# Kernel optimization log

Measured on AMD Instinct MI355X. Metric: run time of the kernel, lower is better.

The kernel has to match this reference:

```python
import jax, jax.numpy as jnp
import numpy as np

B, T, N, M, P, YD = 256, 64, 128, 256, 256, 1


def lstm_cell(x, h, c, Wih, Whh, bih, bhh):
    # torch LSTM gate order: i, f, g, o
    gates = x @ Wih.T + h @ Whh.T + bih + bhh  # (B, 4H)
    i, f, g, o = jnp.split(gates, 4, axis=-1)
    c_new = jax.nn.sigmoid(f) * c + jax.nn.sigmoid(i) * jnp.tanh(g)
    h_new = jax.nn.sigmoid(o) * jnp.tanh(c_new)
    return h_new, c_new


def setup_inputs() -> dict:
    key = jax.random.key(0)
    ks = jax.random.split(key, 20)
    s = 0.05
    return {
        "inputs": jax.random.normal(ks[0], (B, T, N + YD), jnp.float32),
        "WU_e": jax.random.normal(ks[1], (T, 2 * M + T), jnp.float32) * s,
        "v_e": jax.random.normal(ks[2], (1, T), jnp.float32) * s,
        "Wih_e": jax.random.normal(ks[3], (4 * M, N), jnp.float32) * s,
        "Whh_e": jax.random.normal(ks[4], (4 * M, M), jnp.float32) * s,
        "bih_e": jax.random.normal(ks[5], (4 * M,), jnp.float32) * s,
        "bhh_e": jax.random.normal(ks[6], (4 * M,), jnp.float32) * s,
        "WU_d": jax.random.normal(ks[7], (M, 2 * P + M), jnp.float32) * s,
        "v_d": jax.random.normal(ks[8], (1, M), jnp.float32) * s,
        "wb_tilde": jax.random.normal(ks[9], (1, YD + M), jnp.float32) * s,
        "Wih_d": jax.random.normal(ks[10], (4 * P, 1), jnp.float32) * s,
        "Whh_d": jax.random.normal(ks[11], (4 * P, P), jnp.float32) * s,
        "bih_d": jax.random.normal(ks[12], (4 * P,), jnp.float32) * s,
        "bhh_d": jax.random.normal(ks[13], (4 * P,), jnp.float32) * s,
        "Wb_W": jax.random.normal(ks[14], (P, P + M), jnp.float32) * s,
        "Wb_b": jax.random.normal(ks[15], (P,), jnp.float32) * s,
        "vb_W": jax.random.normal(ks[16], (YD, P), jnp.float32) * s,
        "vb_b": jax.random.normal(ks[17], (YD,), jnp.float32) * s,
    }


def _darnn(inputs, WU_e, v_e, Wih_e, Whh_e, bih_e, bhh_e,
           WU_d, v_d, wb_tilde, Wih_d, Whh_d, bih_d, bhh_d,
           Wb_W, Wb_b, vb_W, vb_b):
    X = inputs[:, :, :N]          # (B, T, N)
    Y = inputs[:, :, N:]          # (B, T, YD)
    X_nt = jnp.transpose(X, (0, 2, 1))  # (B, N, T), constant across encoder steps

    # ---------------- Encoder ----------------
    def enc_step(carry, x_t):  # x_t: (B, N)
        h, c = carry
        hs = jnp.concatenate([h, c], axis=-1)  # (B, 2M)
        feat = jnp.concatenate(
            [jnp.broadcast_to(hs[:, None, :], (B, N, 2 * M)), X_nt], axis=-1)  # (B, N, 2M+T)
        E = (jnp.tanh(feat @ WU_e.T) @ v_e.T)[..., 0]  # (B, N)
        alpha = jax.nn.softmax(E, axis=1)
        h, c = lstm_cell(x_t * alpha, h, c, Wih_e, Whh_e, bih_e, bhh_e)
        return (h, c), h

    h0 = jnp.zeros((B, M), inputs.dtype)
    c0 = jnp.zeros((B, M), inputs.dtype)
    _, X_encoded = jax.lax.scan(enc_step, (h0, c0), jnp.transpose(X, (1, 0, 2)))
    Xe_bm = jnp.transpose(X_encoded, (1, 0, 2))  # (B, T, M)

    # ---------------- Decoder ----------------
    def dec_step(carry, y_t):  # y_t: (B, YD)
        h, c, _ = carry
        hs = jnp.concatenate([h, c], axis=-1)  # (B, 2P)
        feat = jnp.concatenate(
            [jnp.broadcast_to(hs[:, None, :], (B, T, 2 * P)), Xe_bm], axis=-1)  # (B, T, 2P+M)
        l = (jnp.tanh(feat @ WU_d.T) @ v_d.T)[..., 0]  # (B, T)
        beta = jax.nn.softmax(l, axis=1)
        ctx = jnp.einsum('bt,btm->bm', beta, Xe_bm)  # (B, M)
        y_tilde = jnp.concatenate([y_t, ctx], axis=-1) @ wb_tilde.T  # (B, 1)
        h, c = lstm_cell(y_tilde, h, c, Wih_d, Whh_d, bih_d, bhh_d)
        return (h, c, ctx), None

    hd0 = jnp.zeros((B, P), inputs.dtype)
    cd0 = jnp.zeros((B, P), inputs.dtype)
    ctx0 = jnp.zeros((B, M), inputs.dtype)
    (h, c, ctx), _ = jax.lax.scan(
        dec_step, (hd0, cd0, ctx0), jnp.transpose(Y[:, :T - 1, :], (1, 0, 2)))

    hidden = jnp.concatenate([h, ctx], axis=-1) @ Wb_W.T + Wb_b  # (B, P)
    y_hat = hidden @ vb_W.T + vb_b  # (B, YD)
    return y_hat


def reference(inputs, WU_e, v_e, Wih_e, Whh_e, bih_e, bhh_e,
              WU_d, v_d, wb_tilde, Wih_d, Whh_d, bih_d, bhh_d,
              Wb_W, Wb_b, vb_W, vb_b):
    return _darnn(inputs, WU_e, v_e, Wih_e, Whh_e, bih_e, bhh_e,
                  WU_d, v_d, wb_tilde, Wih_d, Whh_d, bih_d, bhh_d,
                  Wb_W, Wb_b, vb_W, vb_b)
```

## Files before the change

kernel.cpp:

```cpp
#include <hip/hip_runtime.h>
#include <math.h>


#define OFF_XWT   0u
#define OFF_XEWT  2097152u
#define OFF_XE    6291456u
#define OFF_HE    10485760u
#define OFF_HD    10616832u
#define OFF_SB    10747904u
#define OFF_SDB   10780672u
#define OFF_XA    10911744u
#define OFF_CTX   10944512u
#define OFF_YT    11010048u
#define OFF_BAR   11010304u
#define WS_END    11010816u

#define SLAB_F 24576
#define PER_F  2432
#define SCR_F  12288
#define SMEM_F (SLAB_F + PER_F + SCR_F)
#define SMEM_BYTES (SMEM_F * 4)

__device__ __forceinline__ float fast_tanh(float x) {
  float xc = fminf(15.f, fmaxf(-15.f, x));
  float e = __expf(2.f * xc);
  return 1.f - 2.f * __builtin_amdgcn_rcpf(e + 1.f);
}
__device__ __forceinline__ float fast_sig(float x) {
  float xc = fminf(30.f, fmaxf(-30.f, x));
  return __builtin_amdgcn_rcpf(1.f + __expf(-xc));
}
__device__ __forceinline__ float wave_max(float v) {
#pragma unroll
  for (int o = 32; o; o >>= 1) v = fmaxf(v, __shfl_xor(v, o));
  return v;
}
__device__ __forceinline__ float wave_sum(float v) {
#pragma unroll
  for (int o = 32; o; o >>= 1) v += __shfl_xor(v, o);
  return v;
}
__device__ __forceinline__ float dot4(float4 a, float4 b) {
  return a.x*b.x + a.y*b.y + a.z*b.z + a.w*b.w;
}

__device__ __forceinline__ void st1_sc1(float* p, float v) {
  asm volatile("global_store_dword %0, %1, off sc1" :: "v"(p), "v"(v) : "memory");
}
__device__ __forceinline__ void ld1q_sc1(float4& a, const float* pa) {
  asm volatile("global_load_dwordx4 %0, %1, off sc1\n\ts_waitcnt vmcnt(0)"
               : "=&v"(a) : "v"(pa) : "memory");
}
__device__ __forceinline__ void ld1q_nw(float4& a, const float* pa) {
  asm volatile("global_load_dwordx4 %0, %1, off sc1"
               : "=&v"(a) : "v"(pa) : "memory");
}
__device__ __forceinline__ void vm0() {
  asm volatile("s_waitcnt vmcnt(0)" ::: "memory");
}
__device__ __forceinline__ float ld1s_sc1(const float* p) {
  float v;
  asm volatile("global_load_dword %0, %1, off sc1\n\ts_waitcnt vmcnt(0)"
               : "=&v"(v) : "v"(p) : "memory");
  return v;
}
__device__ __forceinline__ void ld8s_sc1(
    float& a0,float& a1,float& a2,float& a3,float& a4,float& a5,float& a6,float& a7,
    const float* p0,const float* p1,const float* p2,const float* p3,
    const float* p4,const float* p5,const float* p6,const float* p7) {
  asm volatile(
      "global_load_dword %0, %8, off sc1\n\t"
      "global_load_dword %1, %9, off sc1\n\t"
      "global_load_dword %2, %10, off sc1\n\t"
      "global_load_dword %3, %11, off sc1\n\t"
      "global_load_dword %4, %12, off sc1\n\t"
      "global_load_dword %5, %13, off sc1\n\t"
      "global_load_dword %6, %14, off sc1\n\t"
      "global_load_dword %7, %15, off sc1\n\t"
      "s_waitcnt vmcnt(0)"
      : "=&v"(a0),"=&v"(a1),"=&v"(a2),"=&v"(a3),
        "=&v"(a4),"=&v"(a5),"=&v"(a6),"=&v"(a7)
      : "v"(p0),"v"(p1),"v"(p2),"v"(p3),"v"(p4),"v"(p5),"v"(p6),"v"(p7)
      : "memory");
}
__device__ __forceinline__ void atomic_add_sc1(float* p, float v) {
  asm volatile("global_atomic_add_f32 %0, %1, off sc1" :: "v"(p), "v"(v) : "memory");
}

#define FMA16V(a0,a1,a2,a3,xv,wv) \
  a0.x += xv.x*wv.x; a0.y += xv.x*wv.y; a0.z += xv.x*wv.z; a0.w += xv.x*wv.w; \
  a1.x += xv.y*wv.x; a1.y += xv.y*wv.y; a1.z += xv.y*wv.z; a1.w += xv.y*wv.w; \
  a2.x += xv.z*wv.x; a2.y += xv.z*wv.y; a2.z += xv.z*wv.z; a2.w += xv.z*wv.w; \
  a3.x += xv.w*wv.x; a3.y += xv.w*wv.y; a3.z += xv.w*wv.z; a3.w += xv.w*wv.w;

__device__ __forceinline__ void bar_arrive(unsigned* bar) {
  asm volatile("s_waitcnt vmcnt(0)" ::: "memory");
  __syncthreads();
  if (threadIdx.x == 0)
    __hip_atomic_fetch_add(bar, 1u, __ATOMIC_RELAXED, __HIP_MEMORY_SCOPE_AGENT);
}
__device__ __forceinline__ void bar_wait(unsigned* bar, unsigned target) {
  if (threadIdx.x == 0) {
    unsigned cur;
    do {
      cur = __hip_atomic_load(bar, __ATOMIC_RELAXED, __HIP_MEMORY_SCOPE_AGENT);
    } while (cur < target);
  }
  __syncthreads();
}

__global__ void darnn_init(float* __restrict__ ws, float* __restrict__ out) {
  unsigned i = blockIdx.x * 256u + threadIdx.x;
  const unsigned span = WS_END - OFF_HE;
  for (unsigned idx = i; idx < span; idx += gridDim.x * 256u) ws[OFF_HE + idx] = 0.f;
  if (i < 256u) out[i] = 0.f;
}

__global__ __launch_bounds__(512, 2) void darnn_main(
    const float* __restrict__ in,   const float* __restrict__ WUe,   const float* __restrict__ ve,
    const float* __restrict__ Wih_e,const float* __restrict__ Whh_e,
    const float* __restrict__ bih_e,const float* __restrict__ bhh_e,
    const float* __restrict__ WUd,  const float* __restrict__ vd,
    const float* __restrict__ wbt,  const float* __restrict__ Wih_d,
    const float* __restrict__ Whh_d,const float* __restrict__ bih_d, const float* __restrict__ bhh_d,
    const float* __restrict__ WbW,  const float* __restrict__ Wbb,
    const float* __restrict__ vbW,  const float* __restrict__ vbb,
    float* __restrict__ ws, float* __restrict__ out)
{
  extern __shared__ __align__(16) float sm[];
  float* SLAB = sm;
  float* PER  = sm + SLAB_F;
  float* SCR  = sm + SLAB_F + PER_F;
  const int tid = threadIdx.x;
  const int bid = blockIdx.x;
  const int grp = bid >> 4;
  const int mt  = bid & 15;
  const int b0  = grp << 4;

  float* XWt  = ws + OFF_XWT;
  float* XeWt = ws + OFF_XEWT;
  float* Xe   = ws + OFF_XE;
  unsigned* barp = (unsigned*)(ws + OFF_BAR) + grp * 32;
  unsigned barn = 0;

  float* wue_s  = PER;
  float* ve_s   = PER + 2304;
  float* bsum_e = PER + 2368;

  {
    int r = tid & 63, kq = tid >> 6;
    int grow = (r & 3) * 256 + mt * 16 + (r >> 2);
#pragma unroll 4
    for (int q = 0; q < 12; ++q) {
      int k = kq * 48 + q * 4;
      float4 wv = (k < 128) ? *(const float4*)(Wih_e + grow * 128 + k)
                            : *(const float4*)(Whh_e + grow * 256 + (k - 128));
      SLAB[(k + 0) * 64 + r] = wv.x; SLAB[(k + 1) * 64 + r] = wv.y;
      SLAB[(k + 2) * 64 + r] = wv.z; SLAB[(k + 3) * 64 + r] = wv.w;
    }
    {
      int lin = tid * 4;
      int j = lin >> 5, c0 = lin & 31;
      int col = (c0 < 16) ? (mt * 16 + c0) : (256 + mt * 16 + (c0 - 16));
      float4 wv = *(const float4*)(WUe + j * 576 + col);
      *(float4*)(wue_s + j * 36 + c0) = wv;
    }
    if (tid < 64) {
      ve_s[tid] = ve[tid];
      int g = tid >> 4, m2 = tid & 15, m = mt * 16 + m2;
      bsum_e[tid] = bih_e[g * 256 + m] + bhh_e[g * 256 + m];
    }
  }

  {
    float* Xs = SCR;
    const float* Xb = in + bid * 8256;
    __syncthreads();
    for (int it = 0; it < 16; ++it) {
      int lin = tid + it * 512;
      int k = lin >> 7, n = lin & 127;
      Xs[n * 68 + k] = Xb[k * 129 + n];
    }
    __syncthreads();
    int j = tid & 63, nh = tid >> 6;
    float acc[16];
#pragma unroll
    for (int i = 0; i < 16; ++i) acc[i] = 0.f;
    const float* wrow = WUe + j * 576 + 512;
    for (int kc = 0; kc < 4; ++kc) {
      float4 w0 = *(const float4*)(wrow + kc * 16 + 0);
      float4 w1 = *(const float4*)(wrow + kc * 16 + 4);
      float4 w2 = *(const float4*)(wrow + kc * 16 + 8);
      float4 w3 = *(const float4*)(wrow + kc * 16 + 12);
#pragma unroll
      for (int ni = 0; ni < 16; ++ni) {
        const float* xp = Xs + (nh * 16 + ni) * 68 + kc * 16;
        acc[ni] += dot4(*(const float4*)(xp + 0),  w0) + dot4(*(const float4*)(xp + 4),  w1)
                 + dot4(*(const float4*)(xp + 8),  w2) + dot4(*(const float4*)(xp + 12), w3);
      }
    }
    float* dst = XWt + bid * 8192 + j * 128 + nh * 16;
#pragma unroll
    for (int ni = 0; ni < 16; ++ni) dst[ni] = acc[ni];
    __syncthreads();
  }

  float4 whc[8];
#pragma unroll
  for (int q = 0; q < 8; ++q) whc[q] = *(const float4*)(wue_s + (tid & 63) * 36 + q * 4);
  float4 bsE = {0,0,0,0};
  {
    int m2 = tid & 15;
    bsE.x = bsum_e[m2]; bsE.y = bsum_e[16 + m2];
    bsE.z = bsum_e[32 + m2]; bsE.w = bsum_e[48 + m2];
  }
  float xwreg[16];
  {
    int n = tid & 127, jh = tid >> 7;
    const float* xwp = XWt + bid * 8192 + n;
#pragma unroll
    for (int jj = 0; jj < 16; ++jj) xwreg[jj] = xwp[(jh * 16 + jj) << 7];
  }
  float c_reg = 0.f;

  for (int t = 0; t < 64; ++t) {
    const int rd = t & 1, wr2 = (t + 1) & 1;
    float4 h0, h1;
    {
      float* Sj  = SCR;
      float* Eh  = SCR + 64;
      float* r8  = SCR + 576;
      bar_wait(barp, barn);
      {
        int kh = tid >> 2, i4 = (tid & 3) * 4;
        const float* hb = ws + OFF_HE + (unsigned)rd * 65536 + (unsigned)grp * 4096;
        ld1q_nw(h0, hb + kh * 16 + i4);
        ld1q_nw(h1, hb + (128 + kh) * 16 + i4);
        if (tid < 16) {
          float* sp = ws + OFF_SB + (unsigned)rd * 16384 + (unsigned)bid * 64 + tid * 4;
          float4 sv;
          ld1q_sc1(sv, sp);
          st1_sc1(sp + 0, 0.f); st1_sc1(sp + 1, 0.f);
          st1_sc1(sp + 2, 0.f); st1_sc1(sp + 3, 0.f);
          *(float4*)(Sj + tid * 4) = sv;
        }
      }
      __syncthreads();
      {
        int n = tid & 127;
        float e = 0.f;
        int jb = (tid >> 7) * 16;
#pragma unroll
        for (int jj = 0; jj < 16; ++jj)
          e += ve_s[jb + jj] * fast_tanh(xwreg[jj] + Sj[jb + jj]);
        Eh[(tid >> 7) * 128 + n] = e;
      }
      __syncthreads();
      int lane = tid & 63, wid = tid >> 6;
      float En = (tid < 128) ? (Eh[tid] + Eh[128 + tid] + Eh[256 + tid] + Eh[384 + tid]) : -1e30f;
      float mx = wave_max(En);
      if (tid < 128 && lane == 0) r8[wid] = mx;
      __syncthreads();
      mx = fmaxf(r8[0], r8[1]);
      float ex = (tid < 128) ? __expf(En - mx) : 0.f;
      float sw = wave_sum(ex);
      if (tid < 128 && lane == 0) r8[4 + wid] = sw;
      __syncthreads();
      float tot = r8[4] + r8[5];
      if (tid < 128)
        st1_sc1(ws + OFF_XA + (unsigned)grp * 2048 + tid * 16 + mt,
                in[bid * 8256 + t * 129 + tid] * (ex / tot));
    }
    barn += 16;
    bar_arrive(barp);

    {
      float* xah = SCR + 1024;
      float* red = SCR;
      float* hcs = SCR + 10240;
      {
        int kh = tid >> 2, i4 = (tid & 3) * 4;
        *(float4*)(xah + (128 + kh) * 20 + i4) = h0;
        *(float4*)(xah + (256 + kh) * 20 + i4) = h1;
      }
      __syncthreads();
      const int ks = tid >> 6, ml = (tid >> 2) & 15, b4 = tid & 3;
      float4 a0 = {0,0,0,0}, a1 = {0,0,0,0}, a2 = {0,0,0,0}, a3 = {0,0,0,0};
      {
        const float* xp = xah + (unsigned)(128 + ks * 32) * 20 + b4 * 4;
        const float* wp = SLAB + (unsigned)(128 + ks * 32) * 64 + ml * 4;
#pragma unroll 8
        for (int kk = 0; kk < 32; ++kk) {
          float4 xv = *(const float4*)(xp + kk * 20);
          float4 wv = *(const float4*)(wp + kk * 64);
          FMA16V(a0, a1, a2, a3, xv, wv);
        }
      }
      bar_wait(barp, barn);
      {
        int k = tid >> 2, i4 = (tid & 3) * 4;
        float4 q;
        ld1q_sc1(q, ws + OFF_XA + (unsigned)grp * 2048 + k * 16 + i4);
        *(float4*)(xah + k * 20 + i4) = q;
      }
      __syncthreads();
      {
        const float* xp = xah + (unsigned)(ks * 16) * 20 + b4 * 4;
        const float* wp = SLAB + (unsigned)(ks * 16) * 64 + ml * 4;
#pragma unroll 8
        for (int kk = 0; kk < 16; ++kk) {
          float4 xv = *(const float4*)(xp + kk * 20);
          float4 wv = *(const float4*)(wp + kk * 64);
          FMA16V(a0, a1, a2, a3, xv, wv);
        }
      }
      __syncthreads();
      {
        float* rp = red + (unsigned)(ks * 64 + ml * 4 + b4) * 20;
        *(float4*)(rp + 0) = a0; *(float4*)(rp + 4) = a1;
        *(float4*)(rp + 8) = a2; *(float4*)(rp + 12) = a3;
      }
      __syncthreads();
      if (tid < 256) {
        int m2 = tid & 15, bl = tid >> 4;
        int t2 = m2 * 4 + (bl >> 2), bs = bl & 3;
        float4 gate = {0,0,0,0};
#pragma unroll
        for (int k2 = 0; k2 < 8; ++k2) {
          float4 rr = *(const float4*)(red + (unsigned)(k2 * 64 + t2) * 20 + bs * 4);
          gate.x += rr.x; gate.y += rr.y; gate.z += rr.z; gate.w += rr.w;
        }
        float gi = gate.x + bsE.x, gf = gate.y + bsE.y;
        float gg = gate.z + bsE.z, go = gate.w + bsE.w;
        float cn = fast_sig(gf) * c_reg + fast_sig(gi) * fast_tanh(gg);
        float hn = fast_sig(go) * fast_tanh(cn);
        c_reg = cn;
        unsigned m = mt * 16 + m2;
        st1_sc1(ws + OFF_HE + (unsigned)wr2 * 65536 + (unsigned)grp * 4096 + m * 16 + bl, hn);
        st1_sc1(Xe + ((unsigned)(b0 + bl) * 64 + t) * 256 + m, hn);
        hcs[bl * 32 + m2] = hn;
        hcs[bl * 32 + 16 + m2] = cn;
      }
      __syncthreads();
      {
        int j = tid & 63, wq = tid >> 6;
#pragma unroll
        for (int e2 = 0; e2 < 2; ++e2) {
          int bl2 = wq * 2 + e2;
          const float* hp = hcs + bl2 * 32;
          float s = 0.f;
#pragma unroll
          for (int q = 0; q < 4; ++q) {
            s += dot4(*(const float4*)(hp + q * 4), whc[q]);
            s += dot4(*(const float4*)(hp + 16 + q * 4), whc[4 + q]);
          }
          atomic_add_sc1(ws + OFF_SB + (unsigned)wr2 * 16384 + (unsigned)(b0 + bl2) * 64 + j, s);
        }
      }
    }
    barn += 16;
    bar_arrive(barp);
  }
  bar_wait(barp, barn);

  float xe[32];
  {
    int m = tid & 255, half = tid >> 8;
    const float* xb = Xe + (unsigned)bid * 16384 + (unsigned)(half * 32) * 256 + m;
#pragma unroll
    for (int g8 = 0; g8 < 4; ++g8) {
      ld8s_sc1(xe[g8*8+0], xe[g8*8+1], xe[g8*8+2], xe[g8*8+3],
               xe[g8*8+4], xe[g8*8+5], xe[g8*8+6], xe[g8*8+7],
               xb + (g8*8+0)*256, xb + (g8*8+1)*256, xb + (g8*8+2)*256,
               xb + (g8*8+3)*256, xb + (g8*8+4)*256, xb + (g8*8+5)*256,
               xb + (g8*8+6)*256, xb + (g8*8+7)*256);
    }
  }

  float* vd_s   = PER;
  float* wbt_s  = PER + 256;
  float* bsum_d = PER + 520;
  float* wihd_s = PER + 584;
  float* wudT   = SLAB + 16384;
  __syncthreads();
  {
    int r = tid & 63, kq = tid >> 6;
    int grow = (r & 3) * 256 + mt * 16 + (r >> 2);
#pragma unroll 4
    for (int q = 0; q < 8; ++q) {
      int k = kq * 32 + q * 4;
      float4 wv = *(const float4*)(Whh_d + grow * 256 + k);
      SLAB[(k + 0) * 64 + r] = wv.x; SLAB[(k + 1) * 64 + r] = wv.y;
      SLAB[(k + 2) * 64 + r] = wv.z; SLAB[(k + 3) * 64 + r] = wv.w;
    }
    {
      int j = tid & 255, half = tid >> 8;
#pragma unroll
      for (int i = 0; i < 16; ++i) {
        int c = half * 16 + i;
        int col = (c < 16) ? (mt * 16 + c) : (256 + mt * 16 + (c - 16));
        wudT[c * 256 + j] = WUd[(unsigned)j * 768 + col];
      }
    }
    if (tid < 256) vd_s[tid] = vd[tid];
    if (tid < 257) wbt_s[tid] = wbt[tid];
    if (tid < 64) {
      int g = tid >> 4, m2 = tid & 15, m = mt * 16 + m2;
      bsum_d[tid] = bih_d[g * 256 + m] + bhh_d[g * 256 + m];
      wihd_s[tid] = Wih_d[g * 256 + m];
    }
  }
  __syncthreads();

  {
    float* XeT = SCR;
    float* Wdc = SCR + 4096;
    int tt2 = tid & 15, jq = tid >> 4;
    int m = tid & 255, half = tid >> 8, kk_m = m & 63;
    for (int jc = 0; jc < 2; ++jc) {
      float4 c0 = {0,0,0,0}, c1 = {0,0,0,0}, c2 = {0,0,0,0}, c3 = {0,0,0,0};
      for (int kc = 0; kc < 4; ++kc) {
        __syncthreads();
        if ((m >> 6) == kc) {
#pragma unroll
          for (int t4 = 0; t4 < 8; ++t4) {
            float4 v = { xe[t4*4+0], xe[t4*4+1], xe[t4*4+2], xe[t4*4+3] };
            *(float4*)(XeT + kk_m * 64 + half * 32 + t4 * 4) = v;
          }
        }
        {
          int jj = tid >> 2, k16 = (tid & 3) * 16;
          const float* src = WUd + (unsigned)(jc * 128 + jj) * 768 + 512 + kc * 64 + k16;
#pragma unroll
          for (int s4 = 0; s4 < 4; ++s4) {
            float4 wv = *(const float4*)(src + s4 * 4);
            Wdc[(k16 + s4*4 + 0) * 128 + jj] = wv.x;
            Wdc[(k16 + s4*4 + 1) * 128 + jj] = wv.y;
            Wdc[(k16 + s4*4 + 2) * 128 + jj] = wv.z;
            Wdc[(k16 + s4*4 + 3) * 128 + jj] = wv.w;
          }
        }
        __syncthreads();
#pragma unroll 8
        for (int kk = 0; kk < 64; ++kk) {
          float4 xv = *(const float4*)(XeT + kk * 64 + tt2 * 4);
          float4 wv = *(const float4*)(Wdc + kk * 128 + jq * 4);
          FMA16V(c0, c1, c2, c3, wv, xv);
        }
      }
      int jb = jc * 128 + jq * 4;
      *(float4*)(XeWt + ((unsigned)bid * 256 + jb + 0) * 64 + tt2 * 4) = c0;
      *(float4*)(XeWt + ((unsigned)bid * 256 + jb + 1) * 64 + tt2 * 4) = c1;
      *(float4*)(XeWt + ((unsigned)bid * 256 + jb + 2) * 64 + tt2 * 4) = c2;
      *(float4*)(XeWt + ((unsigned)bid * 256 + jb + 3) * 64 + tt2 * 4) = c3;
    }
    __syncthreads();
  }

  float wreg[32];
#pragma unroll
  for (int c = 0; c < 32; ++c) wreg[c] = wudT[c * 256 + (tid & 255)];
  float4 bsD = {0,0,0,0}, wiD = {0,0,0,0};
  {
    int m2 = tid & 15;
    bsD.x = bsum_d[m2]; bsD.y = bsum_d[16 + m2]; bsD.z = bsum_d[32 + m2]; bsD.w = bsum_d[48 + m2];
    wiD.x = wihd_s[m2]; wiD.y = wihd_s[16 + m2]; wiD.z = wihd_s[32 + m2]; wiD.w = wihd_s[48 + m2];
  }
  float xewreg[32];
  {
    int tq = tid & 63, q = tid >> 6;
    const float* xew = XeWt + (unsigned)bid * 16384 + tq;
#pragma unroll
    for (int jj = 0; jj < 32; ++jj) xewreg[jj] = xew[(q * 32 + jj) << 6];
  }
  float cd_reg = 0.f;

  for (int t = 0; t < 63; ++t) {
    const int rd = t & 1, wr2 = (t + 1) & 1;
    float4 h0, h1;
    {
      float* Sdj  = SCR;
      float* lp   = SCR + 256;
      float* beta = SCR + 768;
      float* r8   = SCR + 832;
      float* ctxp = SCR + 840;
      bar_wait(barp, barn);
      {
        int kh = tid >> 2, i4 = (tid & 3) * 4;
        const float* hb = ws + OFF_HD + (unsigned)rd * 65536 + (unsigned)grp * 4096;
        ld1q_nw(h0, hb + kh * 16 + i4);
        ld1q_nw(h1, hb + (128 + kh) * 16 + i4);
        if (tid < 64) {
          float* sp = ws + OFF_SDB + (unsigned)rd * 65536 + (unsigned)bid * 256 + tid * 4;
          float4 sv;
          ld1q_sc1(sv, sp);
          st1_sc1(sp + 0, 0.f); st1_sc1(sp + 1, 0.f);
          st1_sc1(sp + 2, 0.f); st1_sc1(sp + 3, 0.f);
          *(float4*)(Sdj + tid * 4) = sv;
        }
      }
      __syncthreads();
      {
        int tq = tid & 63, q = tid >> 6;
        float l = 0.f;
#pragma unroll 8
        for (int jj = 0; jj < 32; ++jj) {
          int j = q * 32 + jj;
          l += vd_s[j] * fast_tanh(xewreg[jj] + Sdj[j]);
        }
        lp[q * 64 + tq] = l;
      }
      __syncthreads();
      if (tid < 64) {
        float lv = 0.f;
#pragma unroll
        for (int q = 0; q < 8; ++q) lv += lp[q * 64 + tid];
        float mx = wave_max(lv);
        float ex = __expf(lv - mx);
        float sw = wave_sum(ex);
        beta[tid] = ex / sw;
      }
      __syncthreads();
      {
        int m = tid & 255, half = tid >> 8;
        float acc = 0.f;
#pragma unroll
        for (int tt = 0; tt < 32; ++tt) acc += beta[half * 32 + tt] * xe[tt];
        ctxp[half * 256 + m] = acc;
      }
      __syncthreads();
      if (tid < 256) {
        float ctx = ctxp[tid] + ctxp[256 + tid];
        st1_sc1(ws + OFF_CTX + (unsigned)bid * 256 + tid, ctx);
        float yp = ctx * wbt_s[1 + tid];
        float swv = wave_sum(yp);
        int lane = tid & 63, wid = tid >> 6;
        if (lane == 0) r8[wid] = swv;
      }
      __syncthreads();
      if (tid == 0) {
        float yt = wbt_s[0] * in[bid * 8256 + t * 129 + 128] + r8[0] + r8[1] + r8[2] + r8[3];
        st1_sc1(ws + OFF_YT + bid, yt);
      }
    }
    barn += 16;
    bar_arrive(barp);

    {
      float* hT  = SCR + 2048;
      float* red = SCR;
      float* hcs = SCR + 10240;
      {
        int kh = tid >> 2, i4 = (tid & 3) * 4;
        *(float4*)(hT + kh * 20 + i4) = h0;
        *(float4*)(hT + (128 + kh) * 20 + i4) = h1;
      }
      __syncthreads();
      const int ks = tid >> 6, ml = (tid >> 2) & 15, b4 = tid & 3;
      float4 a0 = {0,0,0,0}, a1 = {0,0,0,0}, a2 = {0,0,0,0}, a3 = {0,0,0,0};
      {
        const float* xp = hT + (unsigned)(ks * 32) * 20 + b4 * 4;
        const float* wp = SLAB + (unsigned)(ks * 32) * 64 + ml * 4;
#pragma unroll 8
        for (int kk = 0; kk < 32; ++kk) {
          float4 xv = *(const float4*)(xp + kk * 20);
          float4 wv = *(const float4*)(wp + kk * 64);
          FMA16V(a0, a1, a2, a3, xv, wv);
        }
      }
      __syncthreads();
      {
        float* rp = red + (unsigned)(ks * 64 + ml * 4 + b4) * 20;
        *(float4*)(rp + 0) = a0; *(float4*)(rp + 4) = a1;
        *(float4*)(rp + 8) = a2; *(float4*)(rp + 12) = a3;
      }
      __syncthreads();
      float4 gate = {0,0,0,0};
      if (tid < 256) {
        int m2 = tid & 15, bl = tid >> 4;
        int t2 = m2 * 4 + (bl >> 2), bs = bl & 3;
#pragma unroll
        for (int k2 = 0; k2 < 8; ++k2) {
          float4 rr = *(const float4*)(red + (unsigned)(k2 * 64 + t2) * 20 + bs * 4);
          gate.x += rr.x; gate.y += rr.y; gate.z += rr.z; gate.w += rr.w;
        }
      }
      bar_wait(barp, barn);
      if (tid < 256) {
        int m2 = tid & 15, bl = tid >> 4;
        float yt_reg = ld1s_sc1(ws + OFF_YT + b0 + bl);
        float gi = gate.x + yt_reg * wiD.x + bsD.x;
        float gf = gate.y + yt_reg * wiD.y + bsD.y;
        float gg = gate.z + yt_reg * wiD.z + bsD.z;
        float go = gate.w + yt_reg * wiD.w + bsD.w;
        float cn = fast_sig(gf) * cd_reg + fast_sig(gi) * fast_tanh(gg);
        float hn = fast_sig(go) * fast_tanh(cn);
        cd_reg = cn;
        unsigned m = mt * 16 + m2;
        st1_sc1(ws + OFF_HD + (unsigned)wr2 * 65536 + (unsigned)grp * 4096 + m * 16 + bl, hn);
        hcs[bl * 32 + m2] = hn;
        hcs[bl * 32 + 16 + m2] = cn;
      }
      __syncthreads();
      {
        int j = tid & 255, half = tid >> 8;
#pragma unroll
        for (int e2 = 0; e2 < 8; ++e2) {
          int bl2 = half * 8 + e2;
          const float* hp = hcs + bl2 * 32;
          float s = 0.f;
#pragma unroll
          for (int c = 0; c < 16; ++c) s += hp[c] * wreg[c];
#pragma unroll
          for (int c = 0; c < 16; ++c) s += hp[16 + c] * wreg[16 + c];
          atomic_add_sc1(ws + OFF_SDB + (unsigned)wr2 * 65536 + (unsigned)(b0 + bl2) * 256 + j, s);
        }
      }
    }
    barn += 16;
    bar_arrive(barp);
  }
  bar_wait(barp, barn);

  {
    float* hsf  = SCR;
    float* hid2 = SCR + 8256;
    {
      int l0 = tid * 2, l1 = tid * 2 + 1;
      int k0 = l0 >> 2, i0 = l0 & 3, k1 = l1 >> 2, i1 = l1 & 3;
      const float* hb = ws + OFF_HD + 65536u + (unsigned)grp * 4096;
      int bl0 = l0 >> 6, c0 = (l0 & 63) * 4, bl1 = l1 >> 6, c1 = (l1 & 63) * 4;
      float4 qa, qb, qc, qd;
      ld1q_nw(qa, hb + k0 * 16 + i0 * 4);
      ld1q_nw(qb, hb + k1 * 16 + i1 * 4);
      ld1q_nw(qc, ws + OFF_CTX + (unsigned)(b0 + bl0) * 256 + c0);
      ld1q_nw(qd, ws + OFF_CTX + (unsigned)(b0 + bl1) * 256 + c1);
      vm0();
      hsf[(i0 * 4 + 0) * 516 + k0] = qa.x; hsf[(i0 * 4 + 1) * 516 + k0] = qa.y;
      hsf[(i0 * 4 + 2) * 516 + k0] = qa.z; hsf[(i0 * 4 + 3) * 516 + k0] = qa.w;
      hsf[(i1 * 4 + 0) * 516 + k1] = qb.x; hsf[(i1 * 4 + 1) * 516 + k1] = qb.y;
      hsf[(i1 * 4 + 2) * 516 + k1] = qb.z; hsf[(i1 * 4 + 3) * 516 + k1] = qb.w;
      *(float4*)(hsf + bl0 * 516 + 256 + c0) = qc;
      *(float4*)(hsf + bl1 * 516 + 256 + c1) = qd;
    }
    __syncthreads();
    int bl = tid & 15, p4 = (tid >> 4) & 15, half = tid >> 8;
    int row = mt * 16 + p4;
    const float* wrow = WbW + (unsigned)row * 512 + half * 256;
    const float* hp = hsf + bl * 516 + half * 256;
    float acc = half ? 0.f : Wbb[row];
#pragma unroll 8
    for (int q = 0; q < 64; ++q)
      acc += dot4(*(const float4*)(hp + q * 4), *(const float4*)(wrow + q * 4));
    hid2[half * 272 + bl * 17 + p4] = acc;
    __syncthreads();
    if (tid < 16) {
      float s = 0.f;
#pragma unroll
      for (int p = 0; p < 16; ++p)
        s += (hid2[tid * 17 + p] + hid2[272 + tid * 17 + p]) * vbW[mt * 16 + p];
      if (mt == 0) s += vbb[0];
      atomicAdd(&out[b0 + tid], s);
    }
  }
}

extern "C" void kernel_launch(void* const* d_in, const int* in_sizes, int n_in,
                              void* d_out, int out_size, void* d_ws, size_t ws_size,
                              hipStream_t stream) {
  (void)in_sizes; (void)n_in; (void)out_size; (void)ws_size;
  const float* in    = (const float*)d_in[0];
  const float* WUe   = (const float*)d_in[1];
  const float* ve    = (const float*)d_in[2];
  const float* Wih_e = (const float*)d_in[3];
  const float* Whh_e = (const float*)d_in[4];
  const float* bih_e = (const float*)d_in[5];
  const float* bhh_e = (const float*)d_in[6];
  const float* WUd   = (const float*)d_in[7];
  const float* vd    = (const float*)d_in[8];
  const float* wbt   = (const float*)d_in[9];
  const float* Wih_d = (const float*)d_in[10];
  const float* Whh_d = (const float*)d_in[11];
  const float* bih_d = (const float*)d_in[12];
  const float* bhh_d = (const float*)d_in[13];
  const float* WbW   = (const float*)d_in[14];
  const float* Wbb   = (const float*)d_in[15];
  const float* vbW   = (const float*)d_in[16];
  const float* vbb   = (const float*)d_in[17];
  float* ws  = (float*)d_ws;
  float* out = (float*)d_out;

  (void)hipFuncSetAttribute((const void*)darnn_main,
                            hipFuncAttributeMaxDynamicSharedMemorySize, SMEM_BYTES);
  hipLaunchKernelGGL(darnn_init, dim3(1024), dim3(256), 0, stream, ws, out);
  hipLaunchKernelGGL(darnn_main, dim3(256), dim3(512), SMEM_BYTES, stream,
                     in, WUe, ve, Wih_e, Whh_e, bih_e, bhh_e,
                     WUd, vd, wbt, Wih_d, Whh_d, bih_d, bhh_d,
                     WbW, Wbb, vbW, vbb, ws, out);
}
```

Before: 1.389 ms.

## Specialize warps: attention on half the block, recurrent matvec on the other

In both the encoder and decoder loops, each block is split in two. Threads 0-255 do the attention scores, softmax and context, coordinating through LDS atomic flags instead of block-wide __syncthreads. Threads 256-511 load the previous hidden state and run the h@Whh part of the gate matvec at the same time. The aim is to overlap the attention phase with the recurrent matvec and remove several block barriers per step. In exchange, twice the registers are held per attention thread (xwreg, xe, xewreg) on only half the threads. The spin-polling on LDS flags and the reordered zeroing of score buffers add ordering risk.

```diff
diff --git a/kernel.cpp b/kernel.cpp
--- a/kernel.cpp
+++ b/kernel.cpp
@@ -18,8 +18,14 @@
 #define SLAB_F 24576
 #define PER_F  2432
 #define SCR_F  12288
-#define SMEM_F (SLAB_F + PER_F + SCR_F)
+#define FLG_F  16
+#define SMEM_F (SLAB_F + PER_F + SCR_F + FLG_F)
 #define SMEM_BYTES (SMEM_F * 4)
+
+#define F_E 0
+#define F_L 1
+#define F_B 2
+#define F_Y 3
 
 __device__ __forceinline__ float fast_tanh(float x) {
   float xc = fminf(15.f, fmaxf(-15.f, x));
@@ -57,6 +63,9 @@
 }
 __device__ __forceinline__ void vm0() {
   asm volatile("s_waitcnt vmcnt(0)" ::: "memory");
+}
+__device__ __forceinline__ void lgk0() {
+  asm volatile("s_waitcnt lgkmcnt(0)" ::: "memory");
 }
 __device__ __forceinline__ float ld1s_sc1(const float* p) {
   float v;
@@ -87,6 +96,15 @@
   asm volatile("global_atomic_add_f32 %0, %1, off sc1" :: "v"(p), "v"(v) : "memory");
 }
 
+__device__ __forceinline__ void lds_inc(unsigned* f) {
+  __hip_atomic_fetch_add(f, 1u, __ATOMIC_RELAXED, __HIP_MEMORY_SCOPE_WORKGROUP);
+}
+__device__ __forceinline__ void lds_poll(unsigned* f, unsigned tgt) {
+  unsigned cur;
+  do { cur = __hip_atomic_load(f, __ATOMIC_RELAXED, __HIP_MEMORY_SCOPE_WORKGROUP); } while (cur < tgt);
+  asm volatile("" ::: "memory");
+}
+
 #define FMA16V(a0,a1,a2,a3,xv,wv) \
   a0.x += xv.x*wv.x; a0.y += xv.x*wv.y; a0.z += xv.x*wv.z; a0.w += xv.x*wv.w; \
   a1.x += xv.y*wv.x; a1.y += xv.y*wv.y; a1.z += xv.y*wv.z; a1.w += xv.y*wv.w; \
@@ -131,6 +149,7 @@
   float* SLAB = sm;
   float* PER  = sm + SLAB_F;
   float* SCR  = sm + SLAB_F + PER_F;
+  unsigned* FLG = (unsigned*)(sm + SLAB_F + PER_F + SCR_F);
   const int tid = threadIdx.x;
   const int bid = blockIdx.x;
   const int grp = bid >> 4;
@@ -142,6 +161,8 @@
   float* Xe   = ws + OFF_XE;
   unsigned* barp = (unsigned*)(ws + OFF_BAR) + grp * 32;
   unsigned barn = 0;
+
+  if (tid < FLG_F) FLG[tid] = 0u;
 
   float* wue_s  = PER;
   float* ve_s   = PER + 2304;
@@ -214,161 +235,163 @@
     bsE.x = bsum_e[m2]; bsE.y = bsum_e[16 + m2];
     bsE.z = bsum_e[32 + m2]; bsE.w = bsum_e[48 + m2];
   }
-  float xwreg[16];
-  {
-    int n = tid & 127, jh = tid >> 7;
-    const float* xwp = XWt + bid * 8192 + n;
-#pragma unroll
-    for (int jj = 0; jj < 16; ++jj) xwreg[jj] = xwp[(jh * 16 + jj) << 7];
+  float xwreg[32];
+  if (tid < 256) {
+    int w = tid >> 6, l = tid & 63;
+    const float* xwp = XWt + bid * 8192;
+#pragma unroll
+    for (int jj = 0; jj < 16; ++jj) {
+      xwreg[jj]      = xwp[(w * 16 + jj) * 128 + l];
+      xwreg[16 + jj] = xwp[(w * 16 + jj) * 128 + 64 + l];
+    }
   }
   float c_reg = 0.f;
 
   for (int t = 0; t < 64; ++t) {
     const int rd = t & 1, wr2 = (t + 1) & 1;
-    float4 h0, h1;
+    float* xah = SCR + 1024;
+    const int ks = tid >> 6, ml = (tid >> 2) & 15, b4 = tid & 3;
+    float4 a0 = {0,0,0,0}, a1 = {0,0,0,0}, a2 = {0,0,0,0}, a3 = {0,0,0,0};
+
+    bar_wait(barp, barn);
+
+    if (tid < 256) {
+      int w = tid >> 6, l = tid & 63;
+      float* Sj = SCR;
+      float* Ep = SCR + 64;
+      if (l < 16)
+        Sj[w * 16 + l] = ld1s_sc1(ws + OFF_SB + (unsigned)rd * 16384 + (unsigned)bid * 64 + w * 16 + l);
+      lgk0();
+      float e0 = 0.f, e1 = 0.f;
+#pragma unroll
+      for (int jj = 0; jj < 16; ++jj) {
+        float s = Sj[w * 16 + jj];
+        float vv = ve_s[w * 16 + jj];
+        e0 += vv * fast_tanh(xwreg[jj] + s);
+        e1 += vv * fast_tanh(xwreg[16 + jj] + s);
+      }
+      Ep[w * 128 + l] = e0;
+      Ep[w * 128 + 64 + l] = e1;
+      lgk0();
+      if (l == 0) lds_inc(FLG + F_E);
+      if (w == 0) {
+        lds_poll(FLG + F_E, 4u * (t + 1));
+        float En0 = Ep[l] + Ep[128 + l] + Ep[256 + l] + Ep[384 + l];
+        float En1 = Ep[64 + l] + Ep[192 + l] + Ep[320 + l] + Ep[448 + l];
+        float mx = wave_max(fmaxf(En0, En1));
+        float ex0 = __expf(En0 - mx), ex1 = __expf(En1 - mx);
+        float tot = wave_sum(ex0 + ex1);
+        float rt = __builtin_amdgcn_rcpf(tot);
+        float x0 = in[bid * 8256 + t * 129 + l];
+        float x1 = in[bid * 8256 + t * 129 + 64 + l];
+        float* XAg = ws + OFF_XA + (unsigned)grp * 2048;
+        st1_sc1(XAg + l * 16 + mt, x0 * ex0 * rt);
+        st1_sc1(XAg + (64 + l) * 16 + mt, x1 * ex1 * rt);
+        vm0();
+        if (tid == 0)
+          __hip_atomic_fetch_add(barp, 1u, __ATOMIC_RELAXED, __HIP_MEMORY_SCOPE_AGENT);
+      }
+    } else {
+      int u = tid - 256;
+      float4 h0, h1, h2, h3;
+      const float* hb = ws + OFF_HE + (unsigned)rd * 65536 + (unsigned)grp * 4096 + u * 16;
+      ld1q_nw(h0, hb); ld1q_nw(h1, hb + 4); ld1q_nw(h2, hb + 8); ld1q_nw(h3, hb + 12);
+      vm0();
+      float* row = xah + (unsigned)(128 + u) * 20;
+      *(float4*)(row + 0) = h0; *(float4*)(row + 4) = h1;
+      *(float4*)(row + 8) = h2; *(float4*)(row + 12) = h3;
+      lgk0();
+      int s = u >> 6;
+      const float* xp = xah + (unsigned)(128 + s * 64) * 20 + b4 * 4;
+      const float* wp = SLAB + (unsigned)(128 + s * 64) * 64 + ml * 4;
+#pragma unroll 8
+      for (int kk = 0; kk < 64; ++kk) {
+        float4 xv = *(const float4*)(xp + kk * 20);
+        float4 wv = *(const float4*)(wp + kk * 64);
+        FMA16V(a0, a1, a2, a3, xv, wv);
+      }
+    }
+    barn += 16;
+    __syncthreads();
+    bar_wait(barp, barn);
+
+    if (tid < 16) {
+      float* sp = ws + OFF_SB + (unsigned)rd * 16384 + (unsigned)bid * 64 + tid * 4;
+      st1_sc1(sp + 0, 0.f); st1_sc1(sp + 1, 0.f);
+      st1_sc1(sp + 2, 0.f); st1_sc1(sp + 3, 0.f);
+    }
     {
-      float* Sj  = SCR;
-      float* Eh  = SCR + 64;
-      float* r8  = SCR + 576;
-      bar_wait(barp, barn);
-      {
-        int kh = tid >> 2, i4 = (tid & 3) * 4;
-        const float* hb = ws + OFF_HE + (unsigned)rd * 65536 + (unsigned)grp * 4096;
-        ld1q_nw(h0, hb + kh * 16 + i4);
-        ld1q_nw(h1, hb + (128 + kh) * 16 + i4);
-        if (tid < 16) {
-          float* sp = ws + OFF_SB + (unsigned)rd * 16384 + (unsigned)bid * 64 + tid * 4;
-          float4 sv;
-          ld1q_sc1(sv, sp);
-          st1_sc1(sp + 0, 0.f); st1_sc1(sp + 1, 0.f);
-          st1_sc1(sp + 2, 0.f); st1_sc1(sp + 3, 0.f);
-          *(float4*)(Sj + tid * 4) = sv;
+      int k = tid >> 2, i4 = (tid & 3) * 4;
+      float4 q;
+      ld1q_sc1(q, ws + OFF_XA + (unsigned)grp * 2048 + k * 16 + i4);
+      *(float4*)(xah + k * 20 + i4) = q;
+    }
+    __syncthreads();
+    {
+      const float* xp = xah + (unsigned)(ks * 16) * 20 + b4 * 4;
+      const float* wp = SLAB + (unsigned)(ks * 16) * 64 + ml * 4;
+#pragma unroll 8
+      for (int kk = 0; kk < 16; ++kk) {
+        float4 xv = *(const float4*)(xp + kk * 20);
+        float4 wv = *(const float4*)(wp + kk * 64);
+        FMA16V(a0, a1, a2, a3, xv, wv);
+      }
+    }
+    __syncthreads();
+    float* red = SCR;
+    {
+      float* rp = red + (unsigned)(ks * 64 + ml * 4 + b4) * 20;
+      *(float4*)(rp + 0) = a0; *(float4*)(rp + 4) = a1;
+      *(float4*)(rp + 8) = a2; *(float4*)(rp + 12) = a3;
+    }
+    __syncthreads();
+    float* hcs = SCR + 10240;
+    if (tid < 256) {
+      int m2 = tid & 15, bl = tid >> 4;
+      int t2 = m2 * 4 + (bl >> 2), bs = bl & 3;
+      float4 gate = {0,0,0,0};
+#pragma unroll
+      for (int k2 = 0; k2 < 8; ++k2) {
+        float4 rr = *(const float4*)(red + (unsigned)(k2 * 64 + t2) * 20 + bs * 4);
+        gate.x += rr.x; gate.y += rr.y; gate.z += rr.z; gate.w += rr.w;
+      }
+      float gi = gate.x + bsE.x, gf = gate.y + bsE.y;
+      float gg = gate.z + bsE.z, go = gate.w + bsE.w;
+      float cn = fast_sig(gf) * c_reg + fast_sig(gi) * fast_tanh(gg);
+      float hn = fast_sig(go) * fast_tanh(cn);
+      c_reg = cn;
+      unsigned m = mt * 16 + m2;
+      st1_sc1(ws + OFF_HE + (unsigned)wr2 * 65536 + (unsigned)grp * 4096 + m * 16 + bl, hn);
+      st1_sc1(Xe + ((unsigned)(b0 + bl) * 64 + t) * 256 + m, hn);
+      hcs[bl * 32 + m2] = hn;
+      hcs[bl * 32 + 16 + m2] = cn;
+    }
+    __syncthreads();
+    {
+      int j = tid & 63, wq = tid >> 6;
+#pragma unroll
+      for (int e2 = 0; e2 < 2; ++e2) {
+        int bl2 = wq * 2 + e2;
+        const float* hp = hcs + bl2 * 32;
+        float s = 0.f;
+#pragma unroll
+        for (int q = 0; q < 4; ++q) {
+          s += dot4(*(const float4*)(hp + q * 4), whc[q]);
+          s += dot4(*(const float4*)(hp + 16 + q * 4), whc[4 + q]);
         }
-      }
-      __syncthreads();
-      {
-        int n = tid & 127;
-        float e = 0.f;
-        int jb = (tid >> 7) * 16;
-#pragma unroll
-        for (int jj = 0; jj < 16; ++jj)
-          e += ve_s[jb + jj] * fast_tanh(xwreg[jj] + Sj[jb + jj]);
-        Eh[(tid >> 7) * 128 + n] = e;
-      }
-      __syncthreads();
-      int lane = tid & 63, wid = tid >> 6;
-      float En = (tid < 128) ? (Eh[tid] + Eh[128 + tid] + Eh[256 + tid] + Eh[384 + tid]) : -1e30f;
-      float mx = wave_max(En);
-      if (tid < 128 && lane == 0) r8[wid] = mx;
-      __syncthreads();
-      mx = fmaxf(r8[0], r8[1]);
-      float ex = (tid < 128) ? __expf(En - mx) : 0.f;
-      float sw = wave_sum(ex);
-      if (tid < 128 && lane == 0) r8[4 + wid] = sw;
-      __syncthreads();
-      float tot = r8[4] + r8[5];
-      if (tid < 128)
-        st1_sc1(ws + OFF_XA + (unsigned)grp * 2048 + tid * 16 + mt,
-                in[bid * 8256 + t * 129 + tid] * (ex / tot));
+        atomic_add_sc1(ws + OFF_SB + (unsigned)wr2 * 16384 + (unsigned)(b0 + bl2) * 64 + j, s);
+      }
     }
     barn += 16;
     bar_arrive(barp);
-
-    {
-      float* xah = SCR + 1024;
-      float* red = SCR;
-      float* hcs = SCR + 10240;
-      {
-        int kh = tid >> 2, i4 = (tid & 3) * 4;
-        *(float4*)(xah + (128 + kh) * 20 + i4) = h0;
-        *(float4*)(xah + (256 + kh) * 20 + i4) = h1;
-      }
-      __syncthreads();
-      const int ks = tid >> 6, ml = (tid >> 2) & 15, b4 = tid & 3;
-      float4 a0 = {0,0,0,0}, a1 = {0,0,0,0}, a2 = {0,0,0,0}, a3 = {0,0,0,0};
-      {
-        const float* xp = xah + (unsigned)(128 + ks * 32) * 20 + b4 * 4;
-        const float* wp = SLAB + (unsigned)(128 + ks * 32) * 64 + ml * 4;
-#pragma unroll 8
-        for (int kk = 0; kk < 32; ++kk) {
-          float4 xv = *(const float4*)(xp + kk * 20);
-          float4 wv = *(const float4*)(wp + kk * 64);
-          FMA16V(a0, a1, a2, a3, xv, wv);
-        }
-      }
-      bar_wait(barp, barn);
-      {
-        int k = tid >> 2, i4 = (tid & 3) * 4;
-        float4 q;
-        ld1q_sc1(q, ws + OFF_XA + (unsigned)grp * 2048 + k * 16 + i4);
-        *(float4*)(xah + k * 20 + i4) = q;
-      }
-      __syncthreads();
-      {
-        const float* xp = xah + (unsigned)(ks * 16) * 20 + b4 * 4;
-        const float* wp = SLAB + (unsigned)(ks * 16) * 64 + ml * 4;
-#pragma unroll 8
-        for (int kk = 0; kk < 16; ++kk) {
-          float4 xv = *(const float4*)(xp + kk * 20);
-          float4 wv = *(const float4*)(wp + kk * 64);
-          FMA16V(a0, a1, a2, a3, xv, wv);
-        }
-      }
-      __syncthreads();
-      {
-        float* rp = red + (unsigned)(ks * 64 + ml * 4 + b4) * 20;
-        *(float4*)(rp + 0) = a0; *(float4*)(rp + 4) = a1;
-        *(float4*)(rp + 8) = a2; *(float4*)(rp + 12) = a3;
-      }
-      __syncthreads();
-      if (tid < 256) {
-        int m2 = tid & 15, bl = tid >> 4;
-        int t2 = m2 * 4 + (bl >> 2), bs = bl & 3;
-        float4 gate = {0,0,0,0};
-#pragma unroll
-        for (int k2 = 0; k2 < 8; ++k2) {
-          float4 rr = *(const float4*)(red + (unsigned)(k2 * 64 + t2) * 20 + bs * 4);
-          gate.x += rr.x; gate.y += rr.y; gate.z += rr.z; gate.w += rr.w;
-        }
-        float gi = gate.x + bsE.x, gf = gate.y + bsE.y;
-        float gg = gate.z + bsE.z, go = gate.w + bsE.w;
-        float cn = fast_sig(gf) * c_reg + fast_sig(gi) * fast_tanh(gg);
-        float hn = fast_sig(go) * fast_tanh(cn);
-        c_reg = cn;
-        unsigned m = mt * 16 + m2;
-        st1_sc1(ws + OFF_HE + (unsigned)wr2 * 65536 + (unsigned)grp * 4096 + m * 16 + bl, hn);
-        st1_sc1(Xe + ((unsigned)(b0 + bl) * 64 + t) * 256 + m, hn);
-        hcs[bl * 32 + m2] = hn;
-        hcs[bl * 32 + 16 + m2] = cn;
-      }
-      __syncthreads();
-      {
-        int j = tid & 63, wq = tid >> 6;
-#pragma unroll
-        for (int e2 = 0; e2 < 2; ++e2) {
-          int bl2 = wq * 2 + e2;
-          const float* hp = hcs + bl2 * 32;
-          float s = 0.f;
-#pragma unroll
-          for (int q = 0; q < 4; ++q) {
-            s += dot4(*(const float4*)(hp + q * 4), whc[q]);
-            s += dot4(*(const float4*)(hp + 16 + q * 4), whc[4 + q]);
-          }
-          atomic_add_sc1(ws + OFF_SB + (unsigned)wr2 * 16384 + (unsigned)(b0 + bl2) * 64 + j, s);
-        }
-      }
-    }
-    barn += 16;
-    bar_arrive(barp);
   }
   bar_wait(barp, barn);
 
-  float xe[32];
-  {
-    int m = tid & 255, half = tid >> 8;
-    const float* xb = Xe + (unsigned)bid * 16384 + (unsigned)(half * 32) * 256 + m;
-#pragma unroll
-    for (int g8 = 0; g8 < 4; ++g8) {
+  float xe[64];
+  if (tid < 256) {
+    const float* xb = Xe + (unsigned)bid * 16384 + tid;
+#pragma unroll
+    for (int g8 = 0; g8 < 8; ++g8) {
       ld8s_sc1(xe[g8*8+0], xe[g8*8+1], xe[g8*8+2], xe[g8*8+3],
                xe[g8*8+4], xe[g8*8+5], xe[g8*8+6], xe[g8*8+7],
                xb + (g8*8+0)*256, xb + (g8*8+1)*256, xb + (g8*8+2)*256,
@@ -416,16 +439,16 @@
     float* XeT = SCR;
     float* Wdc = SCR + 4096;
     int tt2 = tid & 15, jq = tid >> 4;
-    int m = tid & 255, half = tid >> 8, kk_m = m & 63;
     for (int jc = 0; jc < 2; ++jc) {
       float4 c0 = {0,0,0,0}, c1 = {0,0,0,0}, c2 = {0,0,0,0}, c3 = {0,0,0,0};
       for (int kc = 0; kc < 4; ++kc) {
         __syncthreads();
-        if ((m >> 6) == kc) {
-#pragma unroll
-          for (int t4 = 0; t4 < 8; ++t4) {
+        if (tid < 256 && (tid >> 6) == kc) {
+          int kk = tid & 63;
+#pragma unroll
+          for (int t4 = 0; t4 < 16; ++t4) {
             float4 v = { xe[t4*4+0], xe[t4*4+1], xe[t4*4+2], xe[t4*4+3] };
-            *(float4*)(XeT + kk_m * 64 + half * 32 + t4 * 4) = v;
+            *(float4*)(XeT + kk * 64 + t4 * 4) = v;
           }
         }
         {
@@ -466,155 +489,141 @@
     bsD.x = bsum_d[m2]; bsD.y = bsum_d[16 + m2]; bsD.z = bsum_d[32 + m2]; bsD.w = bsum_d[48 + m2];
     wiD.x = wihd_s[m2]; wiD.y = wihd_s[16 + m2]; wiD.z = wihd_s[32 + m2]; wiD.w = wihd_s[48 + m2];
   }
-  float xewreg[32];
-  {
-    int tq = tid & 63, q = tid >> 6;
-    const float* xew = XeWt + (unsigned)bid * 16384 + tq;
-#pragma unroll
-    for (int jj = 0; jj < 32; ++jj) xewreg[jj] = xew[(q * 32 + jj) << 6];
+  float xewreg[64];
+  if (tid < 256) {
+    int w = tid >> 6, l = tid & 63;
+    const float* xew = XeWt + (unsigned)bid * 16384 + l;
+#pragma unroll
+    for (int jj = 0; jj < 64; ++jj) xewreg[jj] = xew[(w * 64 + jj) << 6];
   }
   float cd_reg = 0.f;
 
   for (int t = 0; t < 63; ++t) {
     const int rd = t & 1, wr2 = (t + 1) & 1;
-    float4 h0, h1;
-    {
+    const int ml = (tid >> 2) & 15, b4 = tid & 3;
+    float* hT  = SCR + 2048;
+    float* red = SCR + 7168;
+
+    bar_wait(barp, barn);
+
+    if (tid < 256) {
+      int w = tid >> 6, l = tid & 63;
       float* Sdj  = SCR;
       float* lp   = SCR + 256;
-      float* beta = SCR + 768;
-      float* r8   = SCR + 832;
-      float* ctxp = SCR + 840;
-      bar_wait(barp, barn);
-      {
-        int kh = tid >> 2, i4 = (tid & 3) * 4;
-        const float* hb = ws + OFF_HD + (unsigned)rd * 65536 + (unsigned)grp * 4096;
-        ld1q_nw(h0, hb + kh * 16 + i4);
-        ld1q_nw(h1, hb + (128 + kh) * 16 + i4);
-        if (tid < 64) {
-          float* sp = ws + OFF_SDB + (unsigned)rd * 65536 + (unsigned)bid * 256 + tid * 4;
-          float4 sv;
-          ld1q_sc1(sv, sp);
-          st1_sc1(sp + 0, 0.f); st1_sc1(sp + 1, 0.f);
-          st1_sc1(sp + 2, 0.f); st1_sc1(sp + 3, 0.f);
-          *(float4*)(Sdj + tid * 4) = sv;
-        }
-      }
-      __syncthreads();
-      {
-        int tq = tid & 63, q = tid >> 6;
-        float l = 0.f;
+      float* beta = SCR + 512;
+      float* r8   = SCR + 576;
+      Sdj[w * 64 + l] = ld1s_sc1(ws + OFF_SDB + (unsigned)rd * 65536 + (unsigned)bid * 256 + w * 64 + l);
+      lgk0();
+      float lpar = 0.f;
 #pragma unroll 8
-        for (int jj = 0; jj < 32; ++jj) {
-          int j = q * 32 + jj;
-          l += vd_s[j] * fast_tanh(xewreg[jj] + Sdj[j]);
-        }
-        lp[q * 64 + tq] = l;
-      }
-      __syncthreads();
-      if (tid < 64) {
-        float lv = 0.f;
-#pragma unroll
-        for (int q = 0; q < 8; ++q) lv += lp[q * 64 + tid];
+      for (int jj = 0; jj < 64; ++jj)
+        lpar += vd_s[w * 64 + jj] * fast_tanh(xewreg[jj] + Sdj[w * 64 + jj]);
+      lp[w * 64 + l] = lpar;
+      lgk0();
+      if (l == 0) lds_inc(FLG + F_L);
+      if (w == 0) {
+        lds_poll(FLG + F_L, 4u * (t + 1));
+        float lv = lp[l] + lp[64 + l] + lp[128 + l] + lp[192 + l];
         float mx = wave_max(lv);
         float ex = __expf(lv - mx);
         float sw = wave_sum(ex);
-        beta[tid] = ex / sw;
-      }
-      __syncthreads();
-      {
-        int m = tid & 255, half = tid >> 8;
-        float acc = 0.f;
-#pragma unroll
-        for (int tt = 0; tt < 32; ++tt) acc += beta[half * 32 + tt] * xe[tt];
-        ctxp[half * 256 + m] = acc;
-      }
-      __syncthreads();
-      if (tid < 256) {
-        float ctx = ctxp[tid] + ctxp[256 + tid];
-        st1_sc1(ws + OFF_CTX + (unsigned)bid * 256 + tid, ctx);
-        float yp = ctx * wbt_s[1 + tid];
-        float swv = wave_sum(yp);
-        int lane = tid & 63, wid = tid >> 6;
-        if (lane == 0) r8[wid] = swv;
-      }
-      __syncthreads();
-      if (tid == 0) {
-        float yt = wbt_s[0] * in[bid * 8256 + t * 129 + 128] + r8[0] + r8[1] + r8[2] + r8[3];
-        st1_sc1(ws + OFF_YT + bid, yt);
-      }
+        beta[l] = ex * __builtin_amdgcn_rcpf(sw);
+        lgk0();
+        if (l == 0) lds_inc(FLG + F_B);
+      }
+      lds_poll(FLG + F_B, (unsigned)(t + 1));
+      lgk0();
+      float ctx = 0.f;
+#pragma unroll
+      for (int tt = 0; tt < 64; ++tt) ctx += beta[tt] * xe[tt];
+      st1_sc1(ws + OFF_CTX + (unsigned)bid * 256 + tid, ctx);
+      float yp = ctx * wbt_s[1 + tid];
+      float swv = wave_sum(yp);
+      if (l == 0) r8[w] = swv;
+      lgk0();
+      if (l == 0) lds_inc(FLG + F_Y);
+      if (w == 0) {
+        lds_poll(FLG + F_Y, 4u * (t + 1));
+        if (l == 0) {
+          float yt = wbt_s[0] * in[bid * 8256 + t * 129 + 128] + r8[0] + r8[1] + r8[2] + r8[3];
+          st1_sc1(ws + OFF_YT + bid, yt);
+        }
+        vm0();
+        if (tid == 0)
+          __hip_atomic_fetch_add(barp, 1u, __ATOMIC_RELAXED, __HIP_MEMORY_SCOPE_AGENT);
+      }
+    } else {
+      int u = tid - 256;
+      float4 h0, h1, h2, h3;
+      const float* hb = ws + OFF_HD + (unsigned)rd * 65536 + (unsigned)grp * 4096 + u * 16;
+      ld1q_nw(h0, hb); ld1q_nw(h1, hb + 4); ld1q_nw(h2, hb + 8); ld1q_nw(h3, hb + 12);
+      vm0();
+      float* row = hT + (unsigned)u * 20;
+      *(float4*)(row + 0) = h0; *(float4*)(row + 4) = h1;
+      *(float4*)(row + 8) = h2; *(float4*)(row + 12) = h3;
+      lgk0();
+      int s = u >> 6;
+      float4 a0 = {0,0,0,0}, a1 = {0,0,0,0}, a2 = {0,0,0,0}, a3 = {0,0,0,0};
+      const float* xp = hT + (unsigned)(s * 64) * 20 + b4 * 4;
+      const float* wp = SLAB + (unsigned)(s * 64) * 64 + ml * 4;
+#pragma unroll 8
+      for (int kk = 0; kk < 64; ++kk) {
+        float4 xv = *(const float4*)(xp + kk * 20);
+        float4 wv = *(const float4*)(wp + kk * 64);
+        FMA16V(a0, a1, a2, a3, xv, wv);
+      }
+      float* rp = red + (unsigned)(s * 64 + ml * 4 + b4) * 20;
+      *(float4*)(rp + 0) = a0; *(float4*)(rp + 4) = a1;
+      *(float4*)(rp + 8) = a2; *(float4*)(rp + 12) = a3;
     }
     barn += 16;
-    bar_arrive(barp);
-
+    __syncthreads();
+
+    float4 gate = {0,0,0,0};
+    if (tid < 256) {
+      int m2 = tid & 15, bl = tid >> 4;
+      int t2 = m2 * 4 + (bl >> 2), bs = bl & 3;
+#pragma unroll
+      for (int k2 = 0; k2 < 4; ++k2) {
+        float4 rr = *(const float4*)(red + (unsigned)(k2 * 64 + t2) * 20 + bs * 4);
+        gate.x += rr.x; gate.y += rr.y; gate.z += rr.z; gate.w += rr.w;
+      }
+    }
+    bar_wait(barp, barn);
+    if (tid < 64) {
+      float* sp = ws + OFF_SDB + (unsigned)rd * 65536 + (unsigned)bid * 256 + tid * 4;
+      st1_sc1(sp + 0, 0.f); st1_sc1(sp + 1, 0.f);
+      st1_sc1(sp + 2, 0.f); st1_sc1(sp + 3, 0.f);
+    }
+    float* hcs = SCR;
+    if (tid < 256) {
+      int m2 = tid & 15, bl = tid >> 4;
+      float yt_reg = ld1s_sc1(ws + OFF_YT + b0 + bl);
+      float gi = gate.x + yt_reg * wiD.x + bsD.x;
+      float gf = gate.y + yt_reg * wiD.y + bsD.y;
+      float gg = gate.z + yt_reg * wiD.z + bsD.z;
+      float go = gate.w + yt_reg * wiD.w + bsD.w;
+      float cn = fast_sig(gf) * cd_reg + fast_sig(gi) * fast_tanh(gg);
+      float hn = fast_sig(go) * fast_tanh(cn);
+      cd_reg = cn;
+      unsigned m = mt * 16 + m2;
+      st1_sc1(ws + OFF_HD + (unsigned)wr2 * 65536 + (unsigned)grp * 4096 + m * 16 + bl, hn);
+      hcs[bl * 32 + m2] = hn;
+      hcs[bl * 32 + 16 + m2] = cn;
+    }
+    __syncthreads();
     {
-      float* hT  = SCR + 2048;
-      float* red = SCR;
-      float* hcs = SCR + 10240;
-      {
-        int kh = tid >> 2, i4 = (tid & 3) * 4;
-        *(float4*)(hT + kh * 20 + i4) = h0;
-        *(float4*)(hT + (128 + kh) * 20 + i4) = h1;
-      }
-      __syncthreads();
-      const int ks = tid >> 6, ml = (tid >> 2) & 15, b4 = tid & 3;
-      float4 a0 = {0,0,0,0}, a1 = {0,0,0,0}, a2 = {0,0,0,0}, a3 = {0,0,0,0};
-      {
-        const float* xp = hT + (unsigned)(ks * 32) * 20 + b4 * 4;
-        const float* wp = SLAB + (unsigned)(ks * 32) * 64 + ml * 4;
-#pragma unroll 8
-        for (int kk = 0; kk < 32; ++kk) {
-          float4 xv = *(const float4*)(xp + kk * 20);
-          float4 wv = *(const float4*)(wp + kk * 64);
-          FMA16V(a0, a1, a2, a3, xv, wv);
-        }
-      }
-      __syncthreads();
-      {
-        float* rp = red + (unsigned)(ks * 64 + ml * 4 + b4) * 20;
-        *(float4*)(rp + 0) = a0; *(float4*)(rp + 4) = a1;
-        *(float4*)(rp + 8) = a2; *(float4*)(rp + 12) = a3;
-      }
-      __syncthreads();
-      float4 gate = {0,0,0,0};
-      if (tid < 256) {
-        int m2 = tid & 15, bl = tid >> 4;
-        int t2 = m2 * 4 + (bl >> 2), bs = bl & 3;
-#pragma unroll
-        for (int k2 = 0; k2 < 8; ++k2) {
-          float4 rr = *(const float4*)(red + (unsigned)(k2 * 64 + t2) * 20 + bs * 4);
-          gate.x += rr.x; gate.y += rr.y; gate.z += rr.z; gate.w += rr.w;
-        }
-      }
-      bar_wait(barp, barn);
-      if (tid < 256) {
-        int m2 = tid & 15, bl = tid >> 4;
-        float yt_reg = ld1s_sc1(ws + OFF_YT + b0 + bl);
-        float gi = gate.x + yt_reg * wiD.x + bsD.x;
-        float gf = gate.y + yt_reg * wiD.y + bsD.y;
-        float gg = gate.z + yt_reg * wiD.z + bsD.z;
-        float go = gate.w + yt_reg * wiD.w + bsD.w;
-        float cn = fast_sig(gf) * cd_reg + fast_sig(gi) * fast_tanh(gg);
-        float hn = fast_sig(go) * fast_tanh(cn);
-        cd_reg = cn;
-        unsigned m = mt * 16 + m2;
-        st1_sc1(ws + OFF_HD + (unsigned)wr2 * 65536 + (unsigned)grp * 4096 + m * 16 + bl, hn);
-        hcs[bl * 32 + m2] = hn;
-        hcs[bl * 32 + 16 + m2] = cn;
-      }
-      __syncthreads();
-      {
-        int j = tid & 255, half = tid >> 8;
-#pragma unroll
-        for (int e2 = 0; e2 < 8; ++e2) {
-          int bl2 = half * 8 + e2;
-          const float* hp = hcs + bl2 * 32;
-          float s = 0.f;
-#pragma unroll
-          for (int c = 0; c < 16; ++c) s += hp[c] * wreg[c];
-#pragma unroll
-          for (int c = 0; c < 16; ++c) s += hp[16 + c] * wreg[16 + c];
-          atomic_add_sc1(ws + OFF_SDB + (unsigned)wr2 * 65536 + (unsigned)(b0 + bl2) * 256 + j, s);
-        }
+      int j = tid & 255, half = tid >> 8;
+#pragma unroll
+      for (int e2 = 0; e2 < 8; ++e2) {
+        int bl2 = half * 8 + e2;
+        const float* hp = hcs + bl2 * 32;
+        float s = 0.f;
+#pragma unroll
+        for (int c = 0; c < 16; ++c) s += hp[c] * wreg[c];
+#pragma unroll
+        for (int c = 0; c < 16; ++c) s += hp[16 + c] * wreg[16 + c];
+        atomic_add_sc1(ws + OFF_SDB + (unsigned)wr2 * 65536 + (unsigned)(b0 + bl2) * 256 + j, s);
       }
     }
     barn += 16;
```

After: 1.329 ms. 1.05x faster.
